# Optimization experiments

Measured on AMD Instinct MI355X. Metric: run time of the kernel, lower is better.

The kernel has to match this reference:

```python
import jax, jax.numpy as jnp
import numpy as np

B, N, D, H, DH, G = 4, 16384, 256, 8, 64, 64  # batch, tokens, dim, heads, dim_head, slice_num
INNER = H * DH

def _gelu(t):
    return jax.nn.gelu(t, approximate=False)  # torch nn.GELU default is exact erf

def setup_inputs() -> dict:
    key = jax.random.key(0)
    ks = jax.random.split(key, 12)
    s = lambda k, shape, sc: jax.random.normal(k, shape, jnp.float32) * sc
    return {
        "x": jax.random.normal(ks[0], (B, N, D), jnp.float32),
        "Wx": s(ks[1], (INNER, D), 0.05), "bx": jnp.zeros((INNER,), jnp.float32),
        "W1": s(ks[2], (G, DH), 0.1), "b1": jnp.zeros((G,), jnp.float32),
        "W2": s(ks[3], (1, G), 0.1), "b2": jnp.zeros((1,), jnp.float32),
        "bias": jnp.full((1, H, 1, 1), 0.5, jnp.float32),
        "Ws": s(ks[4], (G, DH), 0.1), "bs": jnp.zeros((G,), jnp.float32),
        "Wq": s(ks[5], (DH, DH), 0.1),
        "Wk": s(ks[6], (DH, DH), 0.1),
        "Wv": s(ks[7], (DH, DH), 0.1),
        "Wo": s(ks[8], (D, INNER), 0.05), "bo": jnp.zeros((D,), jnp.float32),
        "u": jax.random.uniform(ks[9], (B, H, N, G), jnp.float32),  # gumbel base noise
    }

def reference(x, Wx, bx, W1, b1, W2, b2, bias, Ws, bs, Wq, Wk, Wv, Wo, bo, u):
    b, n, d = x.shape
    h, dh = bias.shape[1], Wq.shape[0]
    # project and split heads: [B,H,N,dh]
    x_mid = (x @ Wx.T + bx).reshape(b, n, h, dh).transpose(0, 2, 1, 3)
    # per-token temperature MLP + learned bias, clamped
    temp = _gelu(_gelu(x_mid @ W1.T + b1) @ W2.T + b2) + bias  # [B,H,N,1]
    temp = jnp.clip(temp, 0.01)
    # gumbel-softmax soft slice routing
    logits = x_mid @ Ws.T + bs                                  # [B,H,N,G]
    gnoise = -jnp.log(-jnp.log(u + 1e-8) + 1e-8)
    slice_w = jax.nn.softmax((logits + gnoise) / temp, axis=-1)  # [B,H,N,G]
    # weighted pooling into slice tokens
    slice_norm = slice_w.sum(axis=2)                             # [B,H,G]
    slice_tok = jnp.einsum('bhnc,bhng->bhgc', x_mid, slice_w)
    slice_tok = slice_tok / (slice_norm + 1e-5)[..., None]       # [B,H,G,dh]
    # attention over the G slice tokens
    q = slice_tok @ Wq.T
    k = slice_tok @ Wk.T
    v = slice_tok @ Wv.T
    scale = 1.0 / np.sqrt(dh).astype(np.float32)
    attn = jax.nn.softmax(jnp.einsum('bhgc,bhkc->bhgk', q, k) * scale, axis=-1)
    out_s = jnp.einsum('bhgk,bhkc->bhgc', attn, v)               # [B,H,G,dh]
    # scatter back to tokens via slice weights
    out_x = jnp.einsum('bhgc,bhng->bhnc', out_s, slice_w)        # [B,H,N,dh]
    out_x = out_x.transpose(0, 2, 1, 3).reshape(b, n, h * dh)
    return out_x @ Wo.T + bo
```

## Files before the change

kernel.cpp:

```cpp
#include <hip/hip_runtime.h>

constexpr int B_ = 4;
constexpr int N_ = 16384;
constexpr int D_ = 256;
constexpr int H_ = 8;
constexpr int DH_ = 64;
constexpr int G_ = 64;
constexpr int INNER_ = 512;

typedef __attribute__((ext_vector_type(8))) short bf16x8;
typedef __attribute__((ext_vector_type(4))) float f32x4;

__device__ __forceinline__ unsigned short f2bu(float f) {
  union { float f; unsigned int u; } v; v.f = f;
  unsigned int r = v.u + 0x7FFFu + ((v.u >> 16) & 1u);
  return (unsigned short)(r >> 16);
}
__device__ __forceinline__ float bu2f(unsigned short h) {
  union { unsigned int u; float f; } v; v.u = ((unsigned int)h) << 16;
  return v.f;
}
__device__ __forceinline__ float gelu_f(float x) {
  const float ax = fabsf(x);
  const float y = ax * 0.70710678118654752440f;
  const float t = 1.0f / fmaf(0.3275911f, y, 1.0f);
  float poly = 1.061405429f;
  poly = fmaf(poly, t, -1.453152027f);
  poly = fmaf(poly, t, 1.421413741f);
  poly = fmaf(poly, t, -0.284496736f);
  poly = fmaf(poly, t, 0.254829592f);
  poly *= t;
  const float e = __expf(-y * y);
  const float E = fmaf(-poly, e, 1.0f);
  return fmaf(0.5f * ax, E, 0.5f * x);
}

__global__ __launch_bounds__(256) void cast_kernel(const float* __restrict__ in,
                                                   unsigned short* __restrict__ o, int n) {
  int i = (blockIdx.x * 256 + threadIdx.x) * 4;
  if (i + 3 < n) {
    float4 v = *reinterpret_cast<const float4*>(&in[i]);
    o[i + 0] = f2bu(v.x);
    o[i + 1] = f2bu(v.y);
    o[i + 2] = f2bu(v.z);
    o[i + 3] = f2bu(v.w);
  }
}

__global__ __launch_bounds__(256) void prep_wrb_kernel(const float* __restrict__ W1,
                                                       const float* __restrict__ Ws,
                                                       unsigned short* __restrict__ WrB) {
  const int i = blockIdx.x * 256 + threadIdx.x;
  if (i < 8192) {
    const int row = i >> 6, col = i & 63;
    const float v = (row < 64) ? W1[row * 64 + col] : Ws[(row - 64) * 64 + col];
    WrB[i] = f2bu(v);
  }
}

template <int MODE>
__global__ __launch_bounds__(256)
void gemm_bt_kernel(const float* __restrict__ Af32,
                    const unsigned short* __restrict__ Abf,
                    const unsigned short* __restrict__ Bt,
                    unsigned short* __restrict__ Cbf,
                    float* __restrict__ Cf32,
                    const float* __restrict__ bias) {
  constexpr int K = (MODE == 0) ? 256 : 512;
  __shared__ unsigned short As[128][72];
  __shared__ unsigned short Bs[128][72];

  const int tid = threadIdx.x;
  const int lane = tid & 63;
  const int wid = tid >> 6;
  const int wm = wid >> 1;
  const int wn = wid & 1;
  const long m0 = (long)blockIdx.x * 128;
  const int n0 = blockIdx.y * 128;

  long aBase = 0, btBase = 0, cBase = 0;
  if constexpr (MODE == 1) {
    const long z = blockIdx.z;
    aBase = z * (long)N_ * 512;
    btBase = z * (long)D_ * 512;
    cBase = z * (long)N_ * D_;
  }

  f32x4 acc[4][4];
#pragma unroll
  for (int m = 0; m < 4; ++m)
#pragma unroll
    for (int n = 0; n < 4; ++n) acc[m][n] = (f32x4){0.f, 0.f, 0.f, 0.f};

  for (int t = 0; t < K / 64; ++t) {
    const int k0 = t * 64;
    if constexpr (MODE == 0) {
#pragma unroll
      for (int i = 0; i < 8; ++i) {
        const int flat = i * 1024 + tid * 4;
        const int r = flat >> 6;
        const int kk = flat & 63;
        const float4 v = *reinterpret_cast<const float4*>(&Af32[(m0 + r) * 256 + k0 + kk]);
        unsigned short tmp[4] = {f2bu(v.x), f2bu(v.y), f2bu(v.z), f2bu(v.w)};
        *reinterpret_cast<unsigned long long*>(&As[r][kk]) =
            *reinterpret_cast<unsigned long long*>(tmp);
      }
    } else {
#pragma unroll
      for (int i = 0; i < 4; ++i) {
        const int flat = i * 2048 + tid * 8;
        const int r = flat >> 6;
        const int kk = flat & 63;
        *reinterpret_cast<int4*>(&As[r][kk]) =
            *reinterpret_cast<const int4*>(&Abf[aBase + (m0 + r) * (long)K + k0 + kk]);
      }
    }
#pragma unroll
    for (int i = 0; i < 4; ++i) {
      const int flat = i * 2048 + tid * 8;
      const int c = flat >> 6;
      const int kk = flat & 63;
      *reinterpret_cast<int4*>(&Bs[c][kk]) =
          *reinterpret_cast<const int4*>(&Bt[btBase + (n0 + c) * (long)K + k0 + kk]);
    }
    __syncthreads();
#pragma unroll
    for (int kk = 0; kk < 2; ++kk) {
      bf16x8 a[4], bb[4];
#pragma unroll
      for (int m = 0; m < 4; ++m)
        a[m] = *reinterpret_cast<const bf16x8*>(
            &As[wm * 64 + m * 16 + (lane & 15)][kk * 32 + (lane >> 4) * 8]);
#pragma unroll
      for (int n = 0; n < 4; ++n)
        bb[n] = *reinterpret_cast<const bf16x8*>(
            &Bs[wn * 64 + n * 16 + (lane & 15)][kk * 32 + (lane >> 4) * 8]);
#pragma unroll
      for (int m = 0; m < 4; ++m)
#pragma unroll
        for (int n = 0; n < 4; ++n)
          acc[m][n] = __builtin_amdgcn_mfma_f32_16x16x32_bf16(a[m], bb[n], acc[m][n], 0, 0, 0);
    }
    __syncthreads();
  }
#pragma unroll
  for (int n = 0; n < 4; ++n) {
    const int c = n0 + wn * 64 + n * 16 + (lane & 15);
    const float bv = bias[c];
#pragma unroll
    for (int m = 0; m < 4; ++m) {
      const long rb = m0 + wm * 64 + m * 16 + ((lane >> 4) << 2);
#pragma unroll
      for (int j = 0; j < 4; ++j) {
        const float val = acc[m][n][j] + bv;
        if constexpr (MODE == 0) {
          Cbf[(rb + j) * 512 + c] = f2bu(val);
        } else {
          Cf32[cBase + (rb + j) * 256 + c] = val;
        }
      }
    }
  }
}

__global__ __launch_bounds__(256)
void routing_fused_kernel(const unsigned short* __restrict__ xmid,
                          const unsigned short* __restrict__ WrB,
                          const float* __restrict__ u,
                          const float* __restrict__ b1,
                          const float* __restrict__ W2,
                          const float* __restrict__ b2,
                          const float* __restrict__ biasH,
                          const float* __restrict__ bs,
                          unsigned short* __restrict__ wout) {
  __shared__ union SM {
    unsigned short As[64][72];
    float hl1[64 * 67];
  } sm;
  __shared__ float hl2[64 * 67];
  __shared__ float cw2[64], cb1[64], cbs[64], cbh[8];
  __shared__ float tempL[64];

  const int tid = threadIdx.x;
  const int lane = tid & 63;
  const int wid = tid >> 6;
  const int wm = wid >> 1;
  const int wn = wid & 1;
  const int q = lane >> 4;
  const int c15 = lane & 15;

  if (tid < 64) {
    cw2[tid] = W2[tid];
    cb1[tid] = b1[tid];
    cbs[tid] = bs[tid];
  }
  if (tid < 8) cbh[tid] = biasH[tid];
  const float b2g = b2[0];

  bf16x8 bfrag[2][4];
#pragma unroll
  for (int kk = 0; kk < 2; ++kk)
#pragma unroll
    for (int n = 0; n < 4; ++n)
      bfrag[kk][n] = *reinterpret_cast<const bf16x8*>(
          WrB + (wn * 64 + n * 16 + c15) * 64 + kk * 32 + q * 8);

  const unsigned short* Ablk = xmid + (long)blockIdx.x * 4096;
#pragma unroll
  for (int i = 0; i < 2; ++i) {
    const int idx = i * 256 + tid;
    const int row = idx >> 3;
    const int col = (idx & 7) * 8;
    *reinterpret_cast<int4*>(&sm.As[row][col]) = *reinterpret_cast<const int4*>(Ablk + idx * 8);
  }
  __syncthreads();

  f32x4 acc[2][4];
#pragma unroll
  for (int m = 0; m < 2; ++m)
#pragma unroll
    for (int n = 0; n < 4; ++n) acc[m][n] = (f32x4){0.f, 0.f, 0.f, 0.f};

#pragma unroll
  for (int kk = 0; kk < 2; ++kk) {
    bf16x8 a[2];
#pragma unroll
    for (int m = 0; m < 2; ++m)
      a[m] = *reinterpret_cast<const bf16x8*>(
          &sm.As[wm * 32 + m * 16 + c15][kk * 32 + q * 8]);
#pragma unroll
    for (int m = 0; m < 2; ++m)
#pragma unroll
      for (int n = 0; n < 4; ++n)
        acc[m][n] = __builtin_amdgcn_mfma_f32_16x16x32_bf16(a[m], bfrag[kk][n], acc[m][n], 0, 0, 0);
  }
  __syncthreads();

  {
    float bv[4];
    float* dst = (wn == 0) ? sm.hl1 : hl2;
    const float* bsrc = (wn == 0) ? cb1 : cbs;
#pragma unroll
    for (int n = 0; n < 4; ++n) bv[n] = bsrc[n * 16 + c15];
#pragma unroll
    for (int m = 0; m < 2; ++m) {
      const int rb = wm * 32 + m * 16 + q * 4;
#pragma unroll
      for (int n = 0; n < 4; ++n) {
        const int c = n * 16 + c15;
#pragma unroll
        for (int j = 0; j < 4; ++j)
          dst[(rb + j) * 67 + c] = acc[m][n][j] + bv[n];
      }
    }
  }
  __syncthreads();

  const int r_e = tid >> 2;
  const int quarter = tid & 3;
  const int g0 = quarter * 16;
  const long t_e = (long)blockIdx.x * 64 + r_e;
  const int h_e = (int)(t_e & 7);

  float sdot = 0.f;
#pragma unroll
  for (int j = 0; j < 16; ++j)
    sdot = fmaf(gelu_f(sm.hl1[r_e * 67 + g0 + j]), cw2[g0 + j], sdot);
  sdot += __shfl_xor(sdot, 1);
  sdot += __shfl_xor(sdot, 2);
  if (quarter == 0) {
    float temp = gelu_f(sdot + b2g) + cbh[h_e];
    temp = fmaxf(temp, 0.01f);
    tempL[r_e] = 1.0f / temp;
  }
  __syncthreads();

  const long bn_e = t_e >> 3;
  const long b_e = bn_e >> 14;
  const long n_e = bn_e & 16383;
  const long uoff = (((b_e * 8 + h_e) << 14) + n_e) * 64 + g0;

  const float inv_t = tempL[r_e];
  float sv[16];
  float mx = -1e30f;
#pragma unroll
  for (int q8 = 0; q8 < 4; ++q8) {
    const float4 uu = *reinterpret_cast<const float4*>(&u[uoff + q8 * 4]);
    const float ua[4] = {uu.x, uu.y, uu.z, uu.w};
#pragma unroll
    for (int e = 0; e < 4; ++e) {
      const int j = q8 * 4 + e;
      const float gn = -__logf(-__logf(ua[e] + 1e-8f) + 1e-8f);
      const float si = (hl2[r_e * 67 + g0 + j] + gn) * inv_t;
      sv[j] = si;
      mx = fmaxf(mx, si);
    }
  }
  mx = fmaxf(mx, __shfl_xor(mx, 1));
  mx = fmaxf(mx, __shfl_xor(mx, 2));
  float ssum = 0.f;
#pragma unroll
  for (int j = 0; j < 16; ++j) {
    const float e = __expf(sv[j] - mx);
    sv[j] = e;
    ssum += e;
  }
  ssum += __shfl_xor(ssum, 1);
  ssum += __shfl_xor(ssum, 2);
  const float inv_s = 1.0f / ssum;

  unsigned short* wrow = wout + t_e * 64 + g0;
#pragma unroll
  for (int i2 = 0; i2 < 2; ++i2) {
    unsigned short tmp[8];
#pragma unroll
    for (int j = 0; j < 8; ++j) tmp[j] = f2bu(sv[i2 * 8 + j] * inv_s);
    *reinterpret_cast<int4*>(wrow + i2 * 8) = *reinterpret_cast<const int4*>(tmp);
  }
}

__global__ __launch_bounds__(256, 2)
void pool_v2_kernel(const unsigned short* __restrict__ xmid,
                    const unsigned short* __restrict__ wbf,
                    float* __restrict__ pacc, float* __restrict__ pnrm) {
  __shared__ __align__(16) float wl[64][68];
  __shared__ __align__(16) float xl[64][68];
  __shared__ float snl[64];
  const int tid = threadIdx.x;
  const int bx = blockIdx.x;
  const int bh = bx & 31;
  const int chunk = bx >> 5;
  const int b = bh >> 3;
  const int h = bh & 7;
  const int r = tid >> 2;
  const int p = (tid & 3) << 4;
  const int q = tid >> 6;
  const int tin = tid & 63;
  const int gb = ((tin >> 3) & 7) << 3;
  const int cb = (tin & 7) << 3;

  float a[8][8];
#pragma unroll
  for (int gi = 0; gi < 8; ++gi)
#pragma unroll
    for (int ci = 0; ci < 8; ++ci) a[gi][ci] = 0.f;
  float sn[16];
#pragma unroll
  for (int j = 0; j < 16; ++j) sn[j] = 0.f;
  if (tid < 64) snl[tid] = 0.f;

  const long tok0 = (long)b * N_ + chunk * 512;

  for (int sub = 0; sub < 8; ++sub) {
    __syncthreads();
    const long base = (tok0 + sub * 64 + r) * 512 + h * 64 + p;
    const int4 rw0 = *reinterpret_cast<const int4*>(&wbf[base]);
    const int4 rw1 = *reinterpret_cast<const int4*>(&wbf[base + 8]);
    const int4 rx0 = *reinterpret_cast<const int4*>(&xmid[base]);
    const int4 rx1 = *reinterpret_cast<const int4*>(&xmid[base + 8]);
    const unsigned short* pw0 = reinterpret_cast<const unsigned short*>(&rw0);
    const unsigned short* pw1 = reinterpret_cast<const unsigned short*>(&rw1);
    const unsigned short* px0 = reinterpret_cast<const unsigned short*>(&rx0);
    const unsigned short* px1 = reinterpret_cast<const unsigned short*>(&rx1);
#pragma unroll
    for (int j = 0; j < 8; ++j) {
      const float w0 = bu2f(pw0[j]);
      const float w1 = bu2f(pw1[j]);
      wl[r][p + j] = w0;
      wl[r][p + 8 + j] = w1;
      sn[j] += w0;
      sn[8 + j] += w1;
      xl[r][p + j] = bu2f(px0[j]);
      xl[r][p + 8 + j] = bu2f(px1[j]);
    }
    __syncthreads();
    for (int i = 0; i < 16; ++i) {
      const int nn = q * 16 + i;
      const f32x4 w0 = *reinterpret_cast<const f32x4*>(&wl[nn][gb]);
      const f32x4 w1 = *reinterpret_cast<const f32x4*>(&wl[nn][gb + 4]);
      const f32x4 x0 = *reinterpret_cast<const f32x4*>(&xl[nn][cb]);
      const f32x4 x1 = *reinterpret_cast<const f32x4*>(&xl[nn][cb + 4]);
      const float wv[8] = {w0[0], w0[1], w0[2], w0[3], w1[0], w1[1], w1[2], w1[3]};
      const float xv[8] = {x0[0], x0[1], x0[2], x0[3], x1[0], x1[1], x1[2], x1[3]};
#pragma unroll
      for (int gi = 0; gi < 8; ++gi)
#pragma unroll
        for (int ci = 0; ci < 8; ++ci) a[gi][ci] = fmaf(wv[gi], xv[ci], a[gi][ci]);
    }
  }

  __syncthreads();
#pragma unroll
  for (int j = 0; j < 16; ++j) atomicAdd(&snl[p + j], sn[j]);

  float* mA = &wl[0][0];
  float* mB = &xl[0][0];
  __syncthreads();
  if (q == 1 || q == 3) {
    float* mb = (q == 1) ? mA : mB;
#pragma unroll
    for (int gi = 0; gi < 8; ++gi)
#pragma unroll
      for (int ci = 0; ci < 8; ++ci) mb[(gi * 8 + ci) * 64 + tin] = a[gi][ci];
  }
  __syncthreads();
  if (q == 0) {
#pragma unroll
    for (int gi = 0; gi < 8; ++gi)
#pragma unroll
      for (int ci = 0; ci < 8; ++ci) a[gi][ci] += mA[(gi * 8 + ci) * 64 + tin];
  } else if (q == 2) {
#pragma unroll
    for (int gi = 0; gi < 8; ++gi)
#pragma unroll
      for (int ci = 0; ci < 8; ++ci) a[gi][ci] += mB[(gi * 8 + ci) * 64 + tin];
  }
  __syncthreads();
  if (q == 2) {
#pragma unroll
    for (int gi = 0; gi < 8; ++gi)
#pragma unroll
      for (int ci = 0; ci < 8; ++ci) mA[(gi * 8 + ci) * 64 + tin] = a[gi][ci];
  }
  __syncthreads();
  if (q == 0) {
    float* pblk = pacc + (long)bx * 4096;
#pragma unroll
    for (int gi = 0; gi < 8; ++gi) {
      float vals[8];
#pragma unroll
      for (int ci = 0; ci < 8; ++ci) vals[ci] = a[gi][ci] + mA[(gi * 8 + ci) * 64 + tin];
      *reinterpret_cast<float4*>(&pblk[(gb + gi) * 64 + cb]) =
          *reinterpret_cast<const float4*>(&vals[0]);
      *reinterpret_cast<float4*>(&pblk[(gb + gi) * 64 + cb + 4]) =
          *reinterpret_cast<const float4*>(&vals[4]);
    }
  }
  if (tid < 64) pnrm[(long)bx * 64 + tid] = snl[tid];
}

__global__ __launch_bounds__(256)
void pool_reduce_kernel(const float* __restrict__ pacc, const float* __restrict__ pnrm,
                        float* __restrict__ sacc, float* __restrict__ snrm) {
  const int bh = blockIdx.x;
  const int tid = threadIdx.x;
  float s[16];
#pragma unroll
  for (int i = 0; i < 16; ++i) s[i] = 0.f;
  for (int c = 0; c < 32; ++c) {
    const float* src = pacc + ((long)(c * 32 + bh)) * 4096 + tid * 16;
#pragma unroll
    for (int i = 0; i < 16; i += 4) {
      const float4 v = *reinterpret_cast<const float4*>(&src[i]);
      s[i] += v.x; s[i + 1] += v.y; s[i + 2] += v.z; s[i + 3] += v.w;
    }
  }
  float* dst = sacc + (long)bh * 4096 + tid * 16;
#pragma unroll
  for (int i = 0; i < 16; i += 4)
    *reinterpret_cast<float4*>(&dst[i]) = make_float4(s[i], s[i + 1], s[i + 2], s[i + 3]);
  if (tid < 64) {
    float t = 0.f;
    for (int c = 0; c < 32; ++c) t += pnrm[((long)(c * 32 + bh)) * 64 + tid];
    snrm[bh * 64 + tid] = t;
  }
}

__global__ __launch_bounds__(256)
void slice_attn_kernel(const float* __restrict__ sacc,
                       const float* __restrict__ snrm,
                       const float* __restrict__ Wq,
                       const float* __restrict__ Wk,
                       const float* __restrict__ Wv,
                       float* __restrict__ outS) {
  __shared__ float st[64][65];
  __shared__ float qq[64][65];
  __shared__ float kk_[64][65];
  __shared__ float vv[64][65];
  __shared__ float at[64][65];
  __shared__ float nrm[64];
  const int tid = threadIdx.x;
  const int bh = blockIdx.x;
  const int lane = tid & 63;
  const int w = tid >> 6;

  if (tid < 64) nrm[tid] = 1.0f / (snrm[bh * 64 + tid] + 1e-5f);
  __syncthreads();
#pragma unroll
  for (int i = 0; i < 16; ++i) {
    const int idx = tid * 16 + i;
    const int gg = idx >> 6;
    const int cc = idx & 63;
    st[gg][cc] = sacc[(long)bh * 4096 + idx] * nrm[gg];
  }
  __syncthreads();
  for (int cc = 0; cc < 16; ++cc) {
    const int c = w * 16 + cc;
    const float* wqr = &Wq[c * 64];
    const float* wkr = &Wk[c * 64];
    const float* wvr = &Wv[c * 64];
    float q0 = 0.f, q1 = 0.f, q2 = 0.f, q3 = 0.f;
    float k0 = 0.f, k1 = 0.f, k2 = 0.f, k3 = 0.f;
    float v0 = 0.f, v1 = 0.f, v2 = 0.f, v3 = 0.f;
#pragma unroll
    for (int j = 0; j < 64; j += 4) {
      const float s0 = st[lane][j], s1 = st[lane][j + 1];
      const float s2 = st[lane][j + 2], s3 = st[lane][j + 3];
      q0 = fmaf(s0, wqr[j], q0); q1 = fmaf(s1, wqr[j + 1], q1);
      q2 = fmaf(s2, wqr[j + 2], q2); q3 = fmaf(s3, wqr[j + 3], q3);
      k0 = fmaf(s0, wkr[j], k0); k1 = fmaf(s1, wkr[j + 1], k1);
      k2 = fmaf(s2, wkr[j + 2], k2); k3 = fmaf(s3, wkr[j + 3], k3);
      v0 = fmaf(s0, wvr[j], v0); v1 = fmaf(s1, wvr[j + 1], v1);
      v2 = fmaf(s2, wvr[j + 2], v2); v3 = fmaf(s3, wvr[j + 3], v3);
    }
    qq[lane][c] = (q0 + q1) + (q2 + q3);
    kk_[lane][c] = (k0 + k1) + (k2 + k3);
    vv[lane][c] = (v0 + v1) + (v2 + v3);
  }
  __syncthreads();
  for (int cc = 0; cc < 16; ++cc) {
    const int k2i = w * 16 + cc;
    float a0 = 0.f, a1 = 0.f, a2 = 0.f, a3 = 0.f;
#pragma unroll
    for (int j = 0; j < 64; j += 4) {
      a0 = fmaf(qq[lane][j], kk_[k2i][j], a0);
      a1 = fmaf(qq[lane][j + 1], kk_[k2i][j + 1], a1);
      a2 = fmaf(qq[lane][j + 2], kk_[k2i][j + 2], a2);
      a3 = fmaf(qq[lane][j + 3], kk_[k2i][j + 3], a3);
    }
    at[lane][k2i] = ((a0 + a1) + (a2 + a3)) * 0.125f;
  }
  __syncthreads();
  if (tid < 64) {
    float m0 = -1e30f, m1 = -1e30f, m2 = -1e30f, m3 = -1e30f;
#pragma unroll
    for (int j = 0; j < 64; j += 4) {
      m0 = fmaxf(m0, at[tid][j]); m1 = fmaxf(m1, at[tid][j + 1]);
      m2 = fmaxf(m2, at[tid][j + 2]); m3 = fmaxf(m3, at[tid][j + 3]);
    }
    const float m = fmaxf(fmaxf(m0, m1), fmaxf(m2, m3));
    float s0 = 0.f, s1 = 0.f, s2 = 0.f, s3 = 0.f;
#pragma unroll
    for (int j = 0; j < 64; j += 4) {
      const float e0 = __expf(at[tid][j] - m);
      const float e1 = __expf(at[tid][j + 1] - m);
      const float e2 = __expf(at[tid][j + 2] - m);
      const float e3 = __expf(at[tid][j + 3] - m);
      at[tid][j] = e0; at[tid][j + 1] = e1; at[tid][j + 2] = e2; at[tid][j + 3] = e3;
      s0 += e0; s1 += e1; s2 += e2; s3 += e3;
    }
    const float inv = 1.0f / ((s0 + s1) + (s2 + s3));
#pragma unroll
    for (int j = 0; j < 64; ++j) at[tid][j] *= inv;
  }
  __syncthreads();
  for (int cc = 0; cc < 16; ++cc) {
    const int c = w * 16 + cc;
    float a0 = 0.f, a1 = 0.f, a2 = 0.f, a3 = 0.f;
#pragma unroll
    for (int j = 0; j < 64; j += 4) {
      a0 = fmaf(at[lane][j], vv[j][c], a0);
      a1 = fmaf(at[lane][j + 1], vv[j + 1][c], a1);
      a2 = fmaf(at[lane][j + 2], vv[j + 2][c], a2);
      a3 = fmaf(at[lane][j + 3], vv[j + 3][c], a3);
    }
    outS[((long)bh * 64 + lane) * 64 + c] = (a0 + a1) + (a2 + a3);
  }
}

__global__ __launch_bounds__(256)
void mt_build_kernel(const float* __restrict__ outS, const float* __restrict__ Wo,
                     unsigned short* __restrict__ MT) {
  const int bd = blockIdx.x;
  const int b = bd >> 8;
  const int d = bd & 255;
  const int tid = threadIdx.x;
#pragma unroll
  for (int it = 0; it < 2; ++it) {
    const int hg = it * 256 + tid;
    const int h = hg >> 6;
    const int g = hg & 63;
    const float* wor = Wo + (long)d * 512 + h * 64;
    const float* os = outS + ((long)(b * 8 + h) * 64 + g) * 64;
    float a0 = 0.f, a1 = 0.f, a2 = 0.f, a3 = 0.f;
#pragma unroll
    for (int c = 0; c < 64; c += 4) {
      a0 = fmaf(os[c], wor[c], a0);
      a1 = fmaf(os[c + 1], wor[c + 1], a1);
      a2 = fmaf(os[c + 2], wor[c + 2], a2);
      a3 = fmaf(os[c + 3], wor[c + 3], a3);
    }
    MT[((long)b * 256 + d) * 512 + hg] = f2bu((a0 + a1) + (a2 + a3));
  }
}

extern "C" void kernel_launch(void* const* d_in, const int* in_sizes, int n_in,
                              void* d_out, int out_size, void* d_ws, size_t ws_size,
                              hipStream_t stream) {
  const float* x = (const float*)d_in[0];
  const float* Wx = (const float*)d_in[1];
  const float* bx = (const float*)d_in[2];
  const float* W1 = (const float*)d_in[3];
  const float* b1 = (const float*)d_in[4];
  const float* W2 = (const float*)d_in[5];
  const float* b2 = (const float*)d_in[6];
  const float* bias = (const float*)d_in[7];
  const float* Ws = (const float*)d_in[8];
  const float* bs = (const float*)d_in[9];
  const float* Wq = (const float*)d_in[10];
  const float* Wk = (const float*)d_in[11];
  const float* Wv = (const float*)d_in[12];
  const float* Wo = (const float*)d_in[13];
  const float* bo = (const float*)d_in[14];
  const float* u = (const float*)d_in[15];
  float* out = (float*)d_out;

  char* ws = (char*)d_ws;
  unsigned short* xmid = (unsigned short*)(ws + 0);
  unsigned short* wbf = (unsigned short*)(ws + 67108864);
  float* sacc = (float*)(ws + 134217728);
  float* snrm = (float*)(ws + 134742016);
  unsigned short* Wxb = (unsigned short*)(ws + 134750208);
  unsigned short* MT = (unsigned short*)(ws + 135012352);
  unsigned short* WrB = (unsigned short*)(ws + 136060928);
  float* pacc = (float*)(ws + 136077312);
  float* pnrm = (float*)(ws + 152854528);
  float* outS = (float*)(ws + 153116672);

  cast_kernel<<<dim3(128), dim3(256), 0, stream>>>(Wx, Wxb, INNER_ * D_);
  prep_wrb_kernel<<<dim3(32), dim3(256), 0, stream>>>(W1, Ws, WrB);
  gemm_bt_kernel<0><<<dim3(512, 4, 1), dim3(256), 0, stream>>>(x, nullptr, Wxb, xmid, nullptr, bx);
  routing_fused_kernel<<<dim3(8192), dim3(256), 0, stream>>>(xmid, WrB, u, b1, W2, b2, bias, bs, wbf);
  pool_v2_kernel<<<dim3(1024), dim3(256), 0, stream>>>(xmid, wbf, pacc, pnrm);
  pool_reduce_kernel<<<dim3(32), dim3(256), 0, stream>>>(pacc, pnrm, sacc, snrm);
  slice_attn_kernel<<<dim3(32), dim3(256), 0, stream>>>(sacc, snrm, Wq, Wk, Wv, outS);
  mt_build_kernel<<<dim3(1024), dim3(256), 0, stream>>>(outS, Wo, MT);
  gemm_bt_kernel<1><<<dim3(128, 2, 4), dim3(256), 0, stream>>>(nullptr, wbf, MT, nullptr, out, bo);
}
```

Baseline: 346.5 us.

## Use direct global-to-LDS loads in GEMM and precast x to bf16

The tiled GEMM now loads its A and B tiles with global_load_lds (direct global-to-LDS DMA) instead of going through registers. For that it drops the padded LDS layout and stores the tiles unpadded at 64-element rows. To keep the first GEMM on the bf16 path, x is cast to bf16 by a separate kernel into workspace memory that is reused later for the routing weights. The aim is to cut register staging and VGPR pressure. In exchange it adds a full extra read and write pass over x, and the unpadded layout may cause LDS bank conflicts on the MFMA fragment reads.

```diff
diff --git a/kernel.cpp b/kernel.cpp
--- a/kernel.cpp
+++ b/kernel.cpp
@@ -60,15 +60,14 @@
 
 template <int MODE>
 __global__ __launch_bounds__(256)
-void gemm_bt_kernel(const float* __restrict__ Af32,
-                    const unsigned short* __restrict__ Abf,
+void gemm_bt_kernel(const unsigned short* __restrict__ Abf,
                     const unsigned short* __restrict__ Bt,
                     unsigned short* __restrict__ Cbf,
                     float* __restrict__ Cf32,
                     const float* __restrict__ bias) {
   constexpr int K = (MODE == 0) ? 256 : 512;
-  __shared__ unsigned short As[128][72];
-  __shared__ unsigned short Bs[128][72];
+  __shared__ unsigned short As[8192];
+  __shared__ unsigned short Bs[8192];
 
   const int tid = threadIdx.x;
   const int lane = tid & 63;
@@ -94,34 +93,17 @@
 
   for (int t = 0; t < K / 64; ++t) {
     const int k0 = t * 64;
-    if constexpr (MODE == 0) {
-#pragma unroll
-      for (int i = 0; i < 8; ++i) {
-        const int flat = i * 1024 + tid * 4;
-        const int r = flat >> 6;
-        const int kk = flat & 63;
-        const float4 v = *reinterpret_cast<const float4*>(&Af32[(m0 + r) * 256 + k0 + kk]);
-        unsigned short tmp[4] = {f2bu(v.x), f2bu(v.y), f2bu(v.z), f2bu(v.w)};
-        *reinterpret_cast<unsigned long long*>(&As[r][kk]) =
-            *reinterpret_cast<unsigned long long*>(tmp);
-      }
-    } else {
-#pragma unroll
-      for (int i = 0; i < 4; ++i) {
-        const int flat = i * 2048 + tid * 8;
-        const int r = flat >> 6;
-        const int kk = flat & 63;
-        *reinterpret_cast<int4*>(&As[r][kk]) =
-            *reinterpret_cast<const int4*>(&Abf[aBase + (m0 + r) * (long)K + k0 + kk]);
-      }
-    }
 #pragma unroll
     for (int i = 0; i < 4; ++i) {
       const int flat = i * 2048 + tid * 8;
-      const int c = flat >> 6;
+      const int r = flat >> 6;
       const int kk = flat & 63;
-      *reinterpret_cast<int4*>(&Bs[c][kk]) =
-          *reinterpret_cast<const int4*>(&Bt[btBase + (n0 + c) * (long)K + k0 + kk]);
+      __builtin_amdgcn_global_load_lds(
+          (const __attribute__((address_space(1))) unsigned int*)(Abf + aBase + (m0 + r) * (long)K + k0 + kk),
+          (__attribute__((address_space(3))) unsigned int*)(As + flat), 16, 0, 0);
+      __builtin_amdgcn_global_load_lds(
+          (const __attribute__((address_space(1))) unsigned int*)(Bt + btBase + (n0 + r) * (long)K + k0 + kk),
+          (__attribute__((address_space(3))) unsigned int*)(Bs + flat), 16, 0, 0);
     }
     __syncthreads();
 #pragma unroll
@@ -130,11 +112,11 @@
 #pragma unroll
       for (int m = 0; m < 4; ++m)
         a[m] = *reinterpret_cast<const bf16x8*>(
-            &As[wm * 64 + m * 16 + (lane & 15)][kk * 32 + (lane >> 4) * 8]);
+            &As[(wm * 64 + m * 16 + (lane & 15)) * 64 + kk * 32 + (lane >> 4) * 8]);
 #pragma unroll
       for (int n = 0; n < 4; ++n)
         bb[n] = *reinterpret_cast<const bf16x8*>(
-            &Bs[wn * 64 + n * 16 + (lane & 15)][kk * 32 + (lane >> 4) * 8]);
+            &Bs[(wn * 64 + n * 16 + (lane & 15)) * 64 + kk * 32 + (lane >> 4) * 8]);
 #pragma unroll
       for (int m = 0; m < 4; ++m)
 #pragma unroll
@@ -626,14 +608,16 @@
   float* pacc = (float*)(ws + 136077312);
   float* pnrm = (float*)(ws + 152854528);
   float* outS = (float*)(ws + 153116672);
+  unsigned short* xbf = (unsigned short*)(ws + 67108864);
 
   cast_kernel<<<dim3(128), dim3(256), 0, stream>>>(Wx, Wxb, INNER_ * D_);
+  cast_kernel<<<dim3(16384), dim3(256), 0, stream>>>(x, xbf, B_ * N_ * D_);
   prep_wrb_kernel<<<dim3(32), dim3(256), 0, stream>>>(W1, Ws, WrB);
-  gemm_bt_kernel<0><<<dim3(512, 4, 1), dim3(256), 0, stream>>>(x, nullptr, Wxb, xmid, nullptr, bx);
+  gemm_bt_kernel<0><<<dim3(512, 4, 1), dim3(256), 0, stream>>>(xbf, Wxb, xmid, nullptr, bx);
   routing_fused_kernel<<<dim3(8192), dim3(256), 0, stream>>>(xmid, WrB, u, b1, W2, b2, bias, bs, wbf);
   pool_v2_kernel<<<dim3(1024), dim3(256), 0, stream>>>(xmid, wbf, pacc, pnrm);
   pool_reduce_kernel<<<dim3(32), dim3(256), 0, stream>>>(pacc, pnrm, sacc, snrm);
   slice_attn_kernel<<<dim3(32), dim3(256), 0, stream>>>(sacc, snrm, Wq, Wk, Wv, outS);
   mt_build_kernel<<<dim3(1024), dim3(256), 0, stream>>>(outS, Wo, MT);
-  gemm_bt_kernel<1><<<dim3(128, 2, 4), dim3(256), 0, stream>>>(nullptr, wbf, MT, nullptr, out, bo);
-}
+  gemm_bt_kernel<1><<<dim3(128, 2, 4), dim3(256), 0, stream>>>(wbf, MT, nullptr, out, bo);
+}
```

Result: no change. 348.4 us (+0.5%).
